# Kernel optimization log

Hardware: AMD Instinct MI355X
Metric: run time of the kernel (lower is better)

The kernel has to match this reference:

```python
import jax, jax.numpy as jnp
import numpy as np

WH, WW, WD = 4, 4, 4
NUM_HEADS = 12


def _relative_coords():
    # (3, N) flattened coords of the 3D window, N = WH*WW*WD
    g = jnp.stack(jnp.meshgrid(jnp.arange(WH), jnp.arange(WW), jnp.arange(WD), indexing='ij'), axis=0)
    flat = g.reshape(3, -1)
    rel = flat[:, :, None] - flat[:, None, :]          # (3, N, N)
    return jnp.transpose(rel, (1, 2, 0)).astype(jnp.float32)  # (N, N, 3)


def setup_inputs() -> dict:
    key = jax.random.key(0)
    ks = jax.random.split(key, 9)
    B_, N, C = 2048, WH * WW * WD, 384
    s = lambda fan: 1.0 / np.sqrt(fan)
    return {
        'x': jax.random.normal(ks[0], (B_, N, C), jnp.float32),
        'qkv_w': jax.random.normal(ks[1], (C, 3 * C), jnp.float32) * s(C),
        'qkv_b': jax.random.normal(ks[2], (3 * C,), jnp.float32) * 0.02,
        'proj_w': jax.random.normal(ks[3], (C, C), jnp.float32) * s(C),
        'proj_b': jax.random.normal(ks[4], (C,), jnp.float32) * 0.02,
        'mlp_w1': jax.random.normal(ks[5], (3, 64), jnp.float32) * s(3),
        'mlp_b1': jax.random.normal(ks[6], (64,), jnp.float32) * 0.02,
        'mlp_w2': jax.random.normal(ks[7], (64, NUM_HEADS), jnp.float32) * s(64),
        'mlp_b2': jax.random.normal(ks[8], (NUM_HEADS,), jnp.float32) * 0.02,
    }


def reference(x, qkv_w, qkv_b, proj_w, proj_b, mlp_w1, mlp_b1, mlp_w2, mlp_b2):
    B_, N, C = x.shape
    H = NUM_HEADS
    hd = C // H
    scale = hd ** -0.5

    qkv = (x @ qkv_w + qkv_b).reshape(B_, N, 3, H, hd)
    q, k, v = qkv[:, :, 0], qkv[:, :, 1], qkv[:, :, 2]   # (B_, N, H, hd)

    # MLP-based relative position bias: (N, N, 3) -> (H, N, N)
    rel = _relative_coords()
    bias = jax.nn.relu(rel @ mlp_w1 + mlp_b1) @ mlp_w2 + mlp_b2  # (N, N, H)
    bias = jnp.transpose(bias, (2, 0, 1))                        # (H, N, N)

    attn = jnp.einsum('bnhd,bmhd->bhnm', q, k) * scale + bias[None]
    attn = jax.nn.softmax(attn, axis=-1)

    out = jnp.einsum('bhnm,bmhd->bnhd', attn, v).reshape(B_, N, C)
    return out @ proj_w + proj_b
```

## Files before the change

kernel.cpp:

```cpp
#include <hip/hip_runtime.h>
#include <stdint.h>

#define SCALE 0.17677669529663687f

typedef __attribute__((ext_vector_type(8))) short short8;
typedef __attribute__((ext_vector_type(4))) float floatx4;

__device__ __forceinline__ unsigned short f2bf(float f) {
    union { float f; unsigned u; } v; v.f = f;
    unsigned r = (v.u + 0x7fffu + ((v.u >> 16) & 1u)) >> 16;
    return (unsigned short)r;
}

__global__ void prep_weights(const float* __restrict__ qkv_w,
                             const float* __restrict__ proj_w,
                             unsigned short* __restrict__ qkv_wt,
                             unsigned short* __restrict__ proj_wt) {
    int i = blockIdx.x * blockDim.x + threadIdx.x;
    const int nq = 1152 * 384;
    const int np = 384 * 384;
    if (i < nq) {
        int r = i / 384, c = i - r * 384;
        qkv_wt[i] = f2bf(qkv_w[c * 1152 + r]);
    } else if (i < nq + np) {
        int o = i - nq;
        int r = o / 384, c = o - r * 384;
        proj_wt[o] = f2bf(proj_w[c * 384 + r]);
    }
}

__global__ void prep_bias(const float* __restrict__ w1, const float* __restrict__ b1,
                          const float* __restrict__ w2, const float* __restrict__ b2,
                          float* __restrict__ bt) {
    int t = blockIdx.x * blockDim.x + threadIdx.x;
    int i = t >> 6, j = t & 63;
    float r0 = (float)((i >> 4) - (j >> 4));
    float r1 = (float)(((i >> 2) & 3) - ((j >> 2) & 3));
    float r2 = (float)((i & 3) - (j & 3));
    float acc[12];
#pragma unroll
    for (int h = 0; h < 12; ++h) acc[h] = b2[h];
    for (int u = 0; u < 64; ++u) {
        float hv = r0 * w1[u] + r1 * w1[64 + u] + r2 * w1[128 + u] + b1[u];
        hv = fmaxf(hv, 0.f);
#pragma unroll
        for (int h = 0; h < 12; ++h) acc[h] += hv * w2[u * 12 + h];
    }
    for (int h = 0; h < 12; ++h) bt[(h << 12) + (i << 6) + j] = acc[h];
}

#define XP  392
#define QKP 40
#define VTP 72
#define PBP 72
#define OSP 72

__launch_bounds__(384, 2)
__global__ void win_attn(const float* __restrict__ x,
                         const unsigned short* __restrict__ qkv_wt,
                         const float* __restrict__ qkv_b,
                         const unsigned short* __restrict__ proj_wt,
                         const float* __restrict__ proj_b,
                         const float* __restrict__ bt,
                         float* __restrict__ out) {
    __shared__ unsigned short xs[64 * XP];
    __shared__ unsigned short ql[2][64 * QKP];
    __shared__ unsigned short kl[2][64 * QKP];
    __shared__ unsigned short vt[2][32 * VTP];
    __shared__ unsigned short pb[2][4][16 * PBP];
    __shared__ unsigned short osl[2][64 * OSP];
    const int tid  = threadIdx.x;
    const int lane = tid & 63;
    const int w    = tid >> 6;
    const int l15  = lane & 15;
    const int quad = lane >> 4;
    const int b    = blockIdx.x;

    const float* xb = x + (size_t)b * (64 * 384);
#pragma unroll
    for (int it = 0; it < 16; ++it) {
        int idx = it * 384 + tid;
        int row = idx / 96;
        int c4  = idx - row * 96;
        const float4 v = *reinterpret_cast<const float4*>(xb + row * 384 + c4 * 4);
        uint2 pk;
        pk.x = (unsigned)f2bf(v.x) | ((unsigned)f2bf(v.y) << 16);
        pk.y = (unsigned)f2bf(v.z) | ((unsigned)f2bf(v.w) << 16);
        *reinterpret_cast<uint2*>(&xs[row * XP + c4 * 4]) = pk;
    }
    __syncthreads();

    const int j3 = w >> 1;
    const int d2 = w & 1;
    const int ntile = (w < 4) ? 5 : 2;
    const int t0    = (w < 4) ? 5 * w : (20 + 2 * (w - 4));

    const floatx4 zf4 = {0.f, 0.f, 0.f, 0.f};
    floatx4 acc2[5][4];
#pragma unroll
    for (int jj = 0; jj < 5; ++jj)
#pragma unroll
        for (int m = 0; m < 4; ++m) acc2[jj][m] = zf4;

#define PROJ_STEP(PP)                                                                   \
    {                                                                                   \
        const int buf_ = (PP) & 1;                                                      \
        short8 a2_[4][2];                                                               \
        _Pragma("unroll")                                                               \
        for (int m = 0; m < 4; ++m)                                                     \
            _Pragma("unroll")                                                           \
            for (int k2 = 0; k2 < 2; ++k2)                                              \
                a2_[m][k2] = *reinterpret_cast<const short8*>(                          \
                    &osl[buf_][(16 * m + l15) * OSP + k2 * 32 + quad * 8]);             \
        _Pragma("unroll")                                                               \
        for (int jj = 0; jj < 5; ++jj)                                                  \
            if (jj < ntile) {                                                           \
                const unsigned short* pw =                                              \
                    proj_wt + (size_t)((t0 + jj) * 16 + l15) * 384 + (PP) * 64;         \
                const short8 b20 = *reinterpret_cast<const short8*>(pw + quad * 8);     \
                const short8 b21 = *reinterpret_cast<const short8*>(pw + 32 + quad * 8);\
                _Pragma("unroll")                                                       \
                for (int m = 0; m < 4; ++m) {                                           \
                    acc2[jj][m] = __builtin_amdgcn_mfma_f32_16x16x32_bf16(              \
                        a2_[m][0], b20, acc2[jj][m], 0, 0, 0);                          \
                    acc2[jj][m] = __builtin_amdgcn_mfma_f32_16x16x32_bf16(              \
                        a2_[m][1], b21, acc2[jj][m], 0, 0, 0);                          \
                }                                                                       \
            }                                                                           \
    }

#pragma unroll 1
    for (int p = 0; p < 6; ++p) {
        floatx4 acc[2][4];
#pragma unroll
        for (int hh = 0; hh < 2; ++hh)
#pragma unroll
            for (int m = 0; m < 4; ++m) acc[hh][m] = zf4;

        int colbase[2];
#pragma unroll
        for (int hh = 0; hh < 2; ++hh)
            colbase[hh] = j3 * 384 + (2 * p + hh) * 32 + d2 * 16;
        const unsigned short* wcol0 = qkv_wt + (size_t)(colbase[0] + l15) * 384;
        const unsigned short* wcol1 = qkv_wt + (size_t)(colbase[1] + l15) * 384;

#pragma unroll
        for (int kk = 0; kk < 12; ++kk) {
            short8 a[4];
#pragma unroll
            for (int m = 0; m < 4; ++m)
                a[m] = *reinterpret_cast<const short8*>(
                    &xs[(16 * m + l15) * XP + kk * 32 + quad * 8]);
            const short8 bf0 = *reinterpret_cast<const short8*>(wcol0 + kk * 32 + quad * 8);
            const short8 bf1 = *reinterpret_cast<const short8*>(wcol1 + kk * 32 + quad * 8);
#pragma unroll
            for (int m = 0; m < 4; ++m) {
                acc[0][m] = __builtin_amdgcn_mfma_f32_16x16x32_bf16(a[m], bf0, acc[0][m], 0, 0, 0);
                acc[1][m] = __builtin_amdgcn_mfma_f32_16x16x32_bf16(a[m], bf1, acc[1][m], 0, 0, 0);
            }
        }
#pragma unroll
        for (int hh = 0; hh < 2; ++hh) {
            const float bc = qkv_b[colbase[hh] + l15];
            if (j3 < 2) {
                unsigned short* dst = (j3 == 0) ? ql[hh] : kl[hh];
#pragma unroll
                for (int m = 0; m < 4; ++m)
#pragma unroll
                    for (int r = 0; r < 4; ++r)
                        dst[(16 * m + quad * 4 + r) * QKP + d2 * 16 + l15] =
                            f2bf(acc[hh][m][r] + bc);
            } else {
#pragma unroll
                for (int m = 0; m < 4; ++m) {
                    uint2 pk;
                    pk.x = (unsigned)f2bf(acc[hh][m][0] + bc) | ((unsigned)f2bf(acc[hh][m][1] + bc) << 16);
                    pk.y = (unsigned)f2bf(acc[hh][m][2] + bc) | ((unsigned)f2bf(acc[hh][m][3] + bc) << 16);
                    *reinterpret_cast<uint2*>(
                        &vt[hh][(d2 * 16 + l15) * VTP + 16 * m + quad * 4]) = pk;
                }
            }
        }
        __syncthreads();

        const int ntask = (w < 4) ? 1 : 2;
#pragma unroll 1
        for (int tk = 0; tk < ntask; ++tk) {
            const int h  = (w < 4) ? 0 : 1;
            const int rb = (w < 4) ? w : ((w - 4) + 2 * tk);
            const int hg = 2 * p + h;

            const short8 aq = *reinterpret_cast<const short8*>(
                &ql[h][(16 * rb + l15) * QKP + quad * 8]);
            floatx4 s4[4];
#pragma unroll
            for (int c = 0; c < 4; ++c) {
                const short8 bk = *reinterpret_cast<const short8*>(
                    &kl[h][(16 * c + l15) * QKP + quad * 8]);
                s4[c] = __builtin_amdgcn_mfma_f32_16x16x32_bf16(aq, bk, zf4, 0, 0, 0);
            }
            const float* bth = bt + ((size_t)hg << 12);
            float rs[4];
#pragma unroll
            for (int r = 0; r < 4; ++r) {
                const int n = 16 * rb + quad * 4 + r;
#pragma unroll
                for (int c = 0; c < 4; ++c)
                    s4[c][r] = s4[c][r] * SCALE + bth[(n << 6) + 16 * c + l15];
                float m0 = fmaxf(fmaxf(s4[0][r], s4[1][r]), fmaxf(s4[2][r], s4[3][r]));
#pragma unroll
                for (int sh = 1; sh < 16; sh <<= 1) m0 = fmaxf(m0, __shfl_xor(m0, sh, 16));
                float p0 = 0.f;
#pragma unroll
                for (int c = 0; c < 4; ++c) {
                    float pv = __expf(s4[c][r] - m0);
                    s4[c][r] = pv;
                    p0 += pv;
                }
#pragma unroll
                for (int sh = 1; sh < 16; sh <<= 1) p0 += __shfl_xor(p0, sh, 16);
                rs[r] = 1.f / p0;
#pragma unroll
                for (int c = 0; c < 4; ++c)
                    pb[h][rb][(quad * 4 + r) * PBP + 16 * c + l15] = f2bf(s4[c][r]);
            }
            short8 ap[2];
#pragma unroll
            for (int kkp = 0; kkp < 2; ++kkp)
                ap[kkp] = *reinterpret_cast<const short8*>(
                    &pb[h][rb][l15 * PBP + kkp * 32 + quad * 8]);
#pragma unroll
            for (int t = 0; t < 2; ++t) {
                floatx4 oacc = zf4;
#pragma unroll
                for (int kkp = 0; kkp < 2; ++kkp) {
                    const short8 bv = *reinterpret_cast<const short8*>(
                        &vt[h][(16 * t + l15) * VTP + kkp * 32 + quad * 8]);
                    oacc = __builtin_amdgcn_mfma_f32_16x16x32_bf16(ap[kkp], bv, oacc, 0, 0, 0);
                }
#pragma unroll
                for (int r = 0; r < 4; ++r)
                    osl[p & 1][(16 * rb + quad * 4 + r) * OSP + h * 32 + 16 * t + l15] =
                        f2bf(oacc[r] * rs[r]);
            }
        }
        if (p >= 1) PROJ_STEP(p - 1);
        __syncthreads();
    }
    PROJ_STEP(5);

    float* ob = out + (size_t)b * (64 * 384);
#pragma unroll
    for (int jj = 0; jj < 5; ++jj)
        if (jj < ntile) {
            const int col = (t0 + jj) * 16 + l15;
            const float pbias = proj_b[col];
#pragma unroll
            for (int m = 0; m < 4; ++m)
#pragma unroll
                for (int r = 0; r < 4; ++r)
                    ob[(16 * m + quad * 4 + r) * 384 + col] = acc2[jj][m][r] + pbias;
        }
#undef PROJ_STEP
}

extern "C" void kernel_launch(void* const* d_in, const int* in_sizes, int n_in,
                              void* d_out, int out_size, void* d_ws, size_t ws_size,
                              hipStream_t stream) {
    const float* x      = (const float*)d_in[0];
    const float* qkv_w  = (const float*)d_in[1];
    const float* qkv_b  = (const float*)d_in[2];
    const float* proj_w = (const float*)d_in[3];
    const float* proj_b = (const float*)d_in[4];
    const float* mlp_w1 = (const float*)d_in[5];
    const float* mlp_b1 = (const float*)d_in[6];
    const float* mlp_w2 = (const float*)d_in[7];
    const float* mlp_b2 = (const float*)d_in[8];
    float* out = (float*)d_out;

    unsigned short* qkv_wt  = (unsigned short*)d_ws;
    unsigned short* proj_wt = qkv_wt + 1152 * 384;
    float*          bt      = (float*)(proj_wt + 384 * 384);

    prep_weights<<<2304, 256, 0, stream>>>(qkv_w, proj_w, qkv_wt, proj_wt);
    prep_bias<<<16, 256, 0, stream>>>(mlp_w1, mlp_b1, mlp_w2, mlp_b2, bt);
    win_attn<<<2048, 384, 0, stream>>>(x, qkv_wt, qkv_b, proj_wt, proj_b, bt, out);
}
```

Measured before the change: 783.0 us.

## Software-pipeline QKV GEMM, attention, and projection across head-pair stages

Double-buffers the q/k/v shared tiles so the QKV projection for head pair p runs in the same barrier interval as attention for pair p-1 and the output projection for pair p-2. This removes one __syncthreads per iteration and lets MFMA-heavy GEMM work overlap with the softmax and attention phases. In exchange it uses more LDS for the doubled q/k/v buffers, which could reduce occupancy at 2 blocks per CU, and raises register pressure.

```diff
diff --git a/kernel.cpp b/kernel.cpp
--- a/kernel.cpp
+++ b/kernel.cpp
@@ -64,9 +64,9 @@
                          const float* __restrict__ bt,
                          float* __restrict__ out) {
     __shared__ unsigned short xs[64 * XP];
-    __shared__ unsigned short ql[2][64 * QKP];
-    __shared__ unsigned short kl[2][64 * QKP];
-    __shared__ unsigned short vt[2][32 * VTP];
+    __shared__ unsigned short ql[2][2][64 * QKP];
+    __shared__ unsigned short kl[2][2][64 * QKP];
+    __shared__ unsigned short vt[2][2][32 * VTP];
     __shared__ unsigned short pb[2][4][16 * PBP];
     __shared__ unsigned short osl[2][64 * OSP];
     const int tid  = threadIdx.x;
@@ -94,6 +94,8 @@
     const int d2 = w & 1;
     const int ntile = (w < 4) ? 5 : 2;
     const int t0    = (w < 4) ? 5 * w : (20 + 2 * (w - 4));
+    const int h0  = (w < 4) ? 0 : 1;
+    const int rb0 = (w < 4) ? w : (w - 4);
 
     const floatx4 zf4 = {0.f, 0.f, 0.f, 0.f};
     floatx4 acc2[5][4];
@@ -129,127 +131,137 @@
             }                                                                           \
     }
 
+#define B23_TASK(H, RB, PP, RBUF)                                                       \
+    {                                                                                   \
+        const int hg_ = 2 * (PP) + (H);                                                 \
+        const short8 aq_ = *reinterpret_cast<const short8*>(                            \
+            &ql[RBUF][H][(16 * (RB) + l15) * QKP + quad * 8]);                          \
+        floatx4 s4_[4];                                                                 \
+        _Pragma("unroll")                                                               \
+        for (int c = 0; c < 4; ++c) {                                                   \
+            const short8 bk_ = *reinterpret_cast<const short8*>(                        \
+                &kl[RBUF][H][(16 * c + l15) * QKP + quad * 8]);                         \
+            s4_[c] = __builtin_amdgcn_mfma_f32_16x16x32_bf16(aq_, bk_, zf4, 0, 0, 0);   \
+        }                                                                               \
+        const float* bth_ = bt + ((size_t)hg_ << 12);                                   \
+        float rs_[4];                                                                   \
+        _Pragma("unroll")                                                               \
+        for (int r = 0; r < 4; ++r) {                                                   \
+            const int n_ = 16 * (RB) + quad * 4 + r;                                    \
+            _Pragma("unroll")                                                           \
+            for (int c = 0; c < 4; ++c)                                                 \
+                s4_[c][r] = s4_[c][r] * SCALE + bth_[(n_ << 6) + 16 * c + l15];         \
+            float m0_ = fmaxf(fmaxf(s4_[0][r], s4_[1][r]), fmaxf(s4_[2][r], s4_[3][r]));\
+            _Pragma("unroll")                                                           \
+            for (int sh = 1; sh < 16; sh <<= 1) m0_ = fmaxf(m0_, __shfl_xor(m0_, sh, 16)); \
+            float p0_ = 0.f;                                                            \
+            _Pragma("unroll")                                                           \
+            for (int c = 0; c < 4; ++c) {                                               \
+                float pv_ = __expf(s4_[c][r] - m0_);                                    \
+                s4_[c][r] = pv_;                                                        \
+                p0_ += pv_;                                                             \
+            }                                                                           \
+            _Pragma("unroll")                                                           \
+            for (int sh = 1; sh < 16; sh <<= 1) p0_ += __shfl_xor(p0_, sh, 16);         \
+            rs_[r] = 1.f / p0_;                                                         \
+            _Pragma("unroll")                                                           \
+            for (int c = 0; c < 4; ++c)                                                 \
+                pb[H][RB][(quad * 4 + r) * PBP + 16 * c + l15] = f2bf(s4_[c][r]);       \
+        }                                                                               \
+        short8 ap_[2];                                                                  \
+        _Pragma("unroll")                                                               \
+        for (int kkp = 0; kkp < 2; ++kkp)                                               \
+            ap_[kkp] = *reinterpret_cast<const short8*>(                                \
+                &pb[H][RB][l15 * PBP + kkp * 32 + quad * 8]);                           \
+        _Pragma("unroll")                                                               \
+        for (int t = 0; t < 2; ++t) {                                                   \
+            floatx4 oacc_ = zf4;                                                        \
+            _Pragma("unroll")                                                           \
+            for (int kkp = 0; kkp < 2; ++kkp) {                                         \
+                const short8 bv_ = *reinterpret_cast<const short8*>(                    \
+                    &vt[RBUF][H][(16 * t + l15) * VTP + kkp * 32 + quad * 8]);          \
+                oacc_ = __builtin_amdgcn_mfma_f32_16x16x32_bf16(ap_[kkp], bv_, oacc_, 0, 0, 0); \
+            }                                                                           \
+            _Pragma("unroll")                                                           \
+            for (int r = 0; r < 4; ++r)                                                 \
+                osl[(PP) & 1][(16 * (RB) + quad * 4 + r) * OSP + (H) * 32 + 16 * t + l15] = \
+                    f2bf(oacc_[r] * rs_[r]);                                            \
+        }                                                                               \
+    }
+
 #pragma unroll 1
     for (int p = 0; p < 6; ++p) {
-        floatx4 acc[2][4];
-#pragma unroll
-        for (int hh = 0; hh < 2; ++hh)
-#pragma unroll
-            for (int m = 0; m < 4; ++m) acc[hh][m] = zf4;
-
-        int colbase[2];
-#pragma unroll
-        for (int hh = 0; hh < 2; ++hh)
-            colbase[hh] = j3 * 384 + (2 * p + hh) * 32 + d2 * 16;
-        const unsigned short* wcol0 = qkv_wt + (size_t)(colbase[0] + l15) * 384;
-        const unsigned short* wcol1 = qkv_wt + (size_t)(colbase[1] + l15) * 384;
-
-#pragma unroll
-        for (int kk = 0; kk < 12; ++kk) {
-            short8 a[4];
-#pragma unroll
-            for (int m = 0; m < 4; ++m)
-                a[m] = *reinterpret_cast<const short8*>(
-                    &xs[(16 * m + l15) * XP + kk * 32 + quad * 8]);
-            const short8 bf0 = *reinterpret_cast<const short8*>(wcol0 + kk * 32 + quad * 8);
-            const short8 bf1 = *reinterpret_cast<const short8*>(wcol1 + kk * 32 + quad * 8);
-#pragma unroll
-            for (int m = 0; m < 4; ++m) {
-                acc[0][m] = __builtin_amdgcn_mfma_f32_16x16x32_bf16(a[m], bf0, acc[0][m], 0, 0, 0);
-                acc[1][m] = __builtin_amdgcn_mfma_f32_16x16x32_bf16(a[m], bf1, acc[1][m], 0, 0, 0);
+        const int ob = p & 1;
+        {
+            floatx4 acc[2][4];
+#pragma unroll
+            for (int hh = 0; hh < 2; ++hh)
+#pragma unroll
+                for (int m = 0; m < 4; ++m) acc[hh][m] = zf4;
+
+            int colbase[2];
+#pragma unroll
+            for (int hh = 0; hh < 2; ++hh)
+                colbase[hh] = j3 * 384 + (2 * p + hh) * 32 + d2 * 16;
+            const unsigned short* wcol0 = qkv_wt + (size_t)(colbase[0] + l15) * 384;
+            const unsigned short* wcol1 = qkv_wt + (size_t)(colbase[1] + l15) * 384;
+
+#pragma unroll
+            for (int kk = 0; kk < 12; ++kk) {
+                short8 a[4];
+#pragma unroll
+                for (int m = 0; m < 4; ++m)
+                    a[m] = *reinterpret_cast<const short8*>(
+                        &xs[(16 * m + l15) * XP + kk * 32 + quad * 8]);
+                const short8 bf0 = *reinterpret_cast<const short8*>(wcol0 + kk * 32 + quad * 8);
+                const short8 bf1 = *reinterpret_cast<const short8*>(wcol1 + kk * 32 + quad * 8);
+#pragma unroll
+                for (int m = 0; m < 4; ++m) {
+                    acc[0][m] = __builtin_amdgcn_mfma_f32_16x16x32_bf16(a[m], bf0, acc[0][m], 0, 0, 0);
+                    acc[1][m] = __builtin_amdgcn_mfma_f32_16x16x32_bf16(a[m], bf1, acc[1][m], 0, 0, 0);
+                }
             }
-        }
-#pragma unroll
-        for (int hh = 0; hh < 2; ++hh) {
-            const float bc = qkv_b[colbase[hh] + l15];
-            if (j3 < 2) {
-                unsigned short* dst = (j3 == 0) ? ql[hh] : kl[hh];
-#pragma unroll
-                for (int m = 0; m < 4; ++m)
-#pragma unroll
-                    for (int r = 0; r < 4; ++r)
-                        dst[(16 * m + quad * 4 + r) * QKP + d2 * 16 + l15] =
-                            f2bf(acc[hh][m][r] + bc);
-            } else {
-#pragma unroll
-                for (int m = 0; m < 4; ++m) {
-                    uint2 pk;
-                    pk.x = (unsigned)f2bf(acc[hh][m][0] + bc) | ((unsigned)f2bf(acc[hh][m][1] + bc) << 16);
-                    pk.y = (unsigned)f2bf(acc[hh][m][2] + bc) | ((unsigned)f2bf(acc[hh][m][3] + bc) << 16);
-                    *reinterpret_cast<uint2*>(
-                        &vt[hh][(d2 * 16 + l15) * VTP + 16 * m + quad * 4]) = pk;
+#pragma unroll
+            for (int hh = 0; hh < 2; ++hh) {
+                const float bc = qkv_b[colbase[hh] + l15];
+                if (j3 < 2) {
+                    unsigned short* dst = (j3 == 0) ? ql[ob][hh] : kl[ob][hh];
+#pragma unroll
+                    for (int m = 0; m < 4; ++m)
+#pragma unroll
+                        for (int r = 0; r < 4; ++r)
+                            dst[(16 * m + quad * 4 + r) * QKP + d2 * 16 + l15] =
+                                f2bf(acc[hh][m][r] + bc);
+                } else {
+#pragma unroll
+                    for (int m = 0; m < 4; ++m) {
+                        uint2 pk;
+                        pk.x = (unsigned)f2bf(acc[hh][m][0] + bc) | ((unsigned)f2bf(acc[hh][m][1] + bc) << 16);
+                        pk.y = (unsigned)f2bf(acc[hh][m][2] + bc) | ((unsigned)f2bf(acc[hh][m][3] + bc) << 16);
+                        *reinterpret_cast<uint2*>(
+                            &vt[ob][hh][(d2 * 16 + l15) * VTP + 16 * m + quad * 4]) = pk;
+                    }
                 }
             }
         }
+        if (p >= 1) {
+            const int rob = ob ^ 1;
+            B23_TASK(h0, rb0, (p - 1), rob);
+            if (w >= 4) B23_TASK(1, (w - 2), (p - 1), rob);
+        }
+        if (p >= 2) PROJ_STEP(p - 2);
         __syncthreads();
-
-        const int ntask = (w < 4) ? 1 : 2;
-#pragma unroll 1
-        for (int tk = 0; tk < ntask; ++tk) {
-            const int h  = (w < 4) ? 0 : 1;
-            const int rb = (w < 4) ? w : ((w - 4) + 2 * tk);
-            const int hg = 2 * p + h;
-
-            const short8 aq = *reinterpret_cast<const short8*>(
-                &ql[h][(16 * rb + l15) * QKP + quad * 8]);
-            floatx4 s4[4];
-#pragma unroll
-            for (int c = 0; c < 4; ++c) {
-                const short8 bk = *reinterpret_cast<const short8*>(
-                    &kl[h][(16 * c + l15) * QKP + quad * 8]);
-                s4[c] = __builtin_amdgcn_mfma_f32_16x16x32_bf16(aq, bk, zf4, 0, 0, 0);
-            }
-            const float* bth = bt + ((size_t)hg << 12);
-            float rs[4];
-#pragma unroll
-            for (int r = 0; r < 4; ++r) {
-                const int n = 16 * rb + quad * 4 + r;
-#pragma unroll
-                for (int c = 0; c < 4; ++c)
-                    s4[c][r] = s4[c][r] * SCALE + bth[(n << 6) + 16 * c + l15];
-                float m0 = fmaxf(fmaxf(s4[0][r], s4[1][r]), fmaxf(s4[2][r], s4[3][r]));
-#pragma unroll
-                for (int sh = 1; sh < 16; sh <<= 1) m0 = fmaxf(m0, __shfl_xor(m0, sh, 16));
-                float p0 = 0.f;
-#pragma unroll
-                for (int c = 0; c < 4; ++c) {
-                    float pv = __expf(s4[c][r] - m0);
-                    s4[c][r] = pv;
-                    p0 += pv;
-                }
-#pragma unroll
-                for (int sh = 1; sh < 16; sh <<= 1) p0 += __shfl_xor(p0, sh, 16);
-                rs[r] = 1.f / p0;
-#pragma unroll
-                for (int c = 0; c < 4; ++c)
-                    pb[h][rb][(quad * 4 + r) * PBP + 16 * c + l15] = f2bf(s4[c][r]);
-            }
-            short8 ap[2];
-#pragma unroll
-            for (int kkp = 0; kkp < 2; ++kkp)
-                ap[kkp] = *reinterpret_cast<const short8*>(
-                    &pb[h][rb][l15 * PBP + kkp * 32 + quad * 8]);
-#pragma unroll
-            for (int t = 0; t < 2; ++t) {
-                floatx4 oacc = zf4;
-#pragma unroll
-                for (int kkp = 0; kkp < 2; ++kkp) {
-                    const short8 bv = *reinterpret_cast<const short8*>(
-                        &vt[h][(16 * t + l15) * VTP + kkp * 32 + quad * 8]);
-                    oacc = __builtin_amdgcn_mfma_f32_16x16x32_bf16(ap[kkp], bv, oacc, 0, 0, 0);
-                }
-#pragma unroll
-                for (int r = 0; r < 4; ++r)
-                    osl[p & 1][(16 * rb + quad * 4 + r) * OSP + h * 32 + 16 * t + l15] =
-                        f2bf(oacc[r] * rs[r]);
-            }
-        }
-        if (p >= 1) PROJ_STEP(p - 1);
+    }
+
+    {
+        B23_TASK(h0, rb0, 5, 1);
+        if (w >= 4) B23_TASK(1, (w - 2), 5, 1);
+        PROJ_STEP(4);
         __syncthreads();
-    }
-    PROJ_STEP(5);
-
-    float* ob = out + (size_t)b * (64 * 384);
+        PROJ_STEP(5);
+    }
+
+    float* ob_ptr = out + (size_t)b * (64 * 384);
 #pragma unroll
     for (int jj = 0; jj < 5; ++jj)
         if (jj < ntile) {
@@ -259,9 +271,10 @@
             for (int m = 0; m < 4; ++m)
 #pragma unroll
                 for (int r = 0; r < 4; ++r)
-                    ob[(16 * m + quad * 4 + r) * 384 + col] = acc2[jj][m][r] + pbias;
+                    ob_ptr[(16 * m + quad * 4 + r) * 384 + col] = acc2[jj][m][r] + pbias;
         }
 #undef PROJ_STEP
+#undef B23_TASK
 }
 
 extern "C" void kernel_launch(void* const* d_in, const int* in_sizes, int n_in,
```

After: 793.3 us. About the same (+1.3%).
